# Kernel optimization log

Hardware: AMD Instinct MI355X
Metric: run time of the kernel (lower is better)

The kernel has to match this reference:

```python
import jax, jax.numpy as jnp
import numpy as np

DIM = 192
HEADS = 4
EPS = 1e-12  # F.normalize default eps


def setup_inputs() -> dict:
    key = jax.random.key(0)
    k0, k1, k2, k3 = jax.random.split(key, 4)
    x = jax.random.normal(k0, (4, DIM, 128, 128), dtype=jnp.float32)
    # qkv 1x1 conv weight: [3*dim, dim, 1, 1] -> stored as [3*dim, dim]
    w_qkv = jax.random.normal(k1, (3 * DIM, DIM), dtype=jnp.float32) * (1.0 / np.sqrt(DIM))
    # depthwise 3x3 conv weight: [3*dim, 1, 3, 3]
    w_dw = jax.random.normal(k2, (3 * DIM, 1, 3, 3), dtype=jnp.float32) * (1.0 / 3.0)
    # project_out 1x1 conv weight: [dim, dim]
    w_proj = jax.random.normal(k3, (DIM, DIM), dtype=jnp.float32) * (1.0 / np.sqrt(DIM))
    # temperature: ones(heads,1,1), requires_grad=False in original
    temperature = jnp.ones((HEADS, 1, 1), dtype=jnp.float32)
    return {"x": x, "w_qkv": w_qkv, "w_dw": w_dw, "w_proj": w_proj,
            "temperature": temperature}


def _l2norm(t):
    # F.normalize(t, dim=-1): t / max(||t||_2, eps)
    n = jnp.sqrt(jnp.sum(t * t, axis=-1, keepdims=True))
    return t / jnp.maximum(n, EPS)


def reference(x, w_qkv, w_dw, w_proj, temperature):
    b, c, h, w = x.shape
    ch = c // HEADS  # channels per head
    # 1x1 conv (no bias) == channel GEMM
    qkv = jnp.einsum('oc,bchw->bohw', w_qkv, x)
    # depthwise 3x3 conv, padding=1, groups=3*dim
    qkv = jax.lax.conv_general_dilated(
        qkv, w_dw, window_strides=(1, 1), padding=((1, 1), (1, 1)),
        dimension_numbers=('NCHW', 'OIHW', 'NCHW'),
        feature_group_count=3 * c)
    q, k, v = jnp.split(qkv, 3, axis=1)
    # b (head ch) h w -> b head ch (h w)
    def rearr(t):
        return t.reshape(b, HEADS, ch, h * w)
    q, k, v = rearr(q), rearr(k), rearr(v)
    q = _l2norm(q)
    k = _l2norm(k)
    # channel-channel attention: [b, head, ch, ch]
    attn = jnp.einsum('bhcn,bhdn->bhcd', q, k) * temperature[None]
    attn = jax.nn.softmax(attn, axis=-1)
    out = jnp.einsum('bhcd,bhdn->bhcn', attn, v)
    out = out.reshape(b, c, h, w)
    out = jnp.einsum('oc,bchw->bohw', w_proj, out)
    return out
```

## Files before the change

kernel.cpp:

```cpp
#include <hip/hip_runtime.h>

typedef unsigned short u16;
typedef float f32x4 __attribute__((ext_vector_type(4)));
typedef __bf16 bf16x8 __attribute__((ext_vector_type(8)));
typedef unsigned short u16x8 __attribute__((ext_vector_type(8)));
typedef unsigned short u16x4 __attribute__((ext_vector_type(4)));

#define DEV static __device__ __forceinline__

#define QS 16448

DEV u16 f2bf(float f) {
  unsigned int u = __float_as_uint(f);
  u += 0x7FFFu + ((u >> 16) & 1u);
  return (u16)(u >> 16);
}
DEV float bf2f(u16 h) { return __uint_as_float(((unsigned int)h) << 16); }

DEV void gload_lds16(const void* g, void* l) {
  __builtin_amdgcn_global_load_lds(
      (__attribute__((address_space(1))) void*)(unsigned long long)g,
      (__attribute__((address_space(3))) void*)l, 16, 0, 0);
}

DEV void vm_wait(int n) {
  switch (n) {
    case 0:  asm volatile("s_waitcnt vmcnt(0)" ::: "memory"); break;
    case 2:  asm volatile("s_waitcnt vmcnt(2)" ::: "memory"); break;
    case 4:  asm volatile("s_waitcnt vmcnt(4)" ::: "memory"); break;
    case 6:  asm volatile("s_waitcnt vmcnt(6)" ::: "memory"); break;
    case 8:  asm volatile("s_waitcnt vmcnt(8)" ::: "memory"); break;
    case 10: asm volatile("s_waitcnt vmcnt(10)" ::: "memory"); break;
    default: asm volatile("s_waitcnt vmcnt(14)" ::: "memory"); break;
  }
}

__global__ __launch_bounds__(256) void convert_w_kernel(
    const float* __restrict__ in, u16* __restrict__ out, int n) {
  int i = blockIdx.x * 256 + threadIdx.x;
  if (i < n) out[i] = f2bf(in[i]);
}

template <bool IN_F32, bool OUT_BF16, int NJT>
__global__ __launch_bounds__(256, 2) void gemm_bt_kernel(
    const void* __restrict__ Av, const u16* __restrict__ B,
    void* __restrict__ Cv, size_t aBatch, int aStride, size_t bBatch,
    size_t cBatch, int ldC) {
  __shared__ __align__(16) char smem[73728];
  char* sA = smem;

  const int tid = threadIdx.x, wave = tid >> 6, lane = tid & 63;
  const int m0 = blockIdx.x * 64, b = blockIdx.y;
  const char* Bbase = (const char*)(B + (size_t)b * bBatch);
  char* bufs = smem + 24576 + wave * 12288;
  const int jwbase = wave * (NJT * 16);
  constexpr int S = OUT_BF16 ? 2 : 4;

  f32x4 vaf[3][4];
  u16x8 vau[2][4];
  if (IN_F32) {
    const float* Xb = (const float*)Av + (size_t)b * aBatch + m0;
    const int cbl = tid & 15, iq = tid >> 4;
#pragma unroll
    for (int p = 0; p < 3; ++p)
#pragma unroll
      for (int r = 0; r < 4; ++r)
        vaf[p][r] = *(const f32x4*)(Xb + (size_t)((p * 16 + cbl) * 4 + r) *
                                             aStride + iq * 4);
  } else {
    const u16* Vb = (const u16*)Av + (size_t)b * aBatch + m0;
#pragma unroll
    for (int p = 0; p < 2; ++p) {
      const int task = p * 256 + tid;
      if (task < 384) {
        const int cb = task >> 3, io = task & 7;
#pragma unroll
        for (int r = 0; r < 4; ++r)
          vau[p][r] = *(const u16x8*)(Vb + (size_t)(cb * 4 + r) * aStride +
                                      io * 8);
      }
    }
  }
#pragma unroll
  for (int t = 0; t < 2; ++t) {
    if (t < NJT) {
#pragma unroll
      for (int i = 0; i < 6; ++i) {
        const int d = i * 1024 + lane * 16;
        const int row = d / 384, inrow = d - row * 384;
        gload_lds16(Bbase + (size_t)(jwbase + t * 16 + row) * 384 +
                        (inrow ^ ((row & 7) << 4)),
                    bufs + t * 6144 + i * 1024);
      }
    }
  }
  if (IN_F32) {
    const int cbl = tid & 15, iq = tid >> 4;
#pragma unroll
    for (int p = 0; p < 3; ++p) {
      const int cb = p * 16 + cbl;
#pragma unroll
      for (int j = 0; j < 4; ++j) {
        const int n = iq * 4 + j;
        u16x4 col;
        col[0] = f2bf(vaf[p][0][j]);
        col[1] = f2bf(vaf[p][1][j]);
        col[2] = f2bf(vaf[p][2][j]);
        col[3] = f2bf(vaf[p][3][j]);
        *(u16x4*)(sA + n * 384 + ((cb * 8) ^ ((n & 7) << 4))) = col;
      }
    }
  } else {
#pragma unroll
    for (int p = 0; p < 2; ++p) {
      const int task = p * 256 + tid;
      if (task < 384) {
        const int cb = task >> 3, io = task & 7;
#pragma unroll
        for (int j = 0; j < 8; ++j) {
          const int n = io * 8 + j;
          u16x4 col;
          col[0] = vau[p][0][j];
          col[1] = vau[p][1][j];
          col[2] = vau[p][2][j];
          col[3] = vau[p][3][j];
          *(u16x4*)(sA + n * 384 + ((cb * 8) ^ ((n & 7) << 4))) = col;
        }
      }
    }
  }
  asm volatile("s_waitcnt lgkmcnt(0)" ::: "memory");
  __builtin_amdgcn_s_barrier();

  const int l15 = lane & 15, lg = lane >> 4;
  const int swm = (l15 & 7) << 4;

  bf16x8 af[4][6];
#pragma unroll
  for (int mi = 0; mi < 4; ++mi)
#pragma unroll
    for (int ks = 0; ks < 6; ++ks)
      af[mi][ks] = *(const bf16x8*)(sA + (mi * 16 + l15) * 384 +
                                    ((ks * 64 + lg * 16) ^ swm));
  asm volatile("s_waitcnt lgkmcnt(0)" ::: "memory");
  __builtin_amdgcn_s_barrier();

  char* rbuf = sA + wave * 6144;

#pragma unroll
  for (int t = 0; t < NJT; ++t) {
    vm_wait(t == 0 ? (NJT > 1 ? 6 : 0) : (S + (t + 1 < NJT ? 6 : 0)));
    __builtin_amdgcn_sched_barrier(0);
    char* bw = bufs + (t & 1) * 6144;
    bf16x8 bfv[6];
#pragma unroll
    for (int ks = 0; ks < 6; ++ks)
      bfv[ks] = *(const bf16x8*)(bw + l15 * 384 + ((ks * 64 + lg * 16) ^ swm));
    f32x4 acc[4];
#pragma unroll
    for (int mi = 0; mi < 4; ++mi) acc[mi] = (f32x4){0.f, 0.f, 0.f, 0.f};
#pragma unroll
    for (int ks = 0; ks < 6; ++ks)
#pragma unroll
      for (int mi = 0; mi < 4; ++mi)
        acc[mi] = __builtin_amdgcn_mfma_f32_16x16x32_bf16(af[mi][ks], bfv[ks],
                                                          acc[mi], 0, 0, 0);
    if (OUT_BF16) {
#pragma unroll
      for (int mi = 0; mi < 4; ++mi) {
        u16x4 ov;
#pragma unroll
        for (int r = 0; r < 4; ++r) ov[r] = f2bf(acc[mi][r]);
        *(u16x4*)(rbuf + l15 * 136 + mi * 32 + lg * 8) = ov;
      }
      asm volatile("s_waitcnt lgkmcnt(0)" ::: "memory");
      u16* Cb = (u16*)Cv + (size_t)b * cBatch;
#pragma unroll
      for (int half = 0; half < 2; ++half) {
        const int row = half * 8 + (lane >> 3);
        const u16x8 val = *(const u16x8*)(rbuf + row * 136 + (lane & 7) * 16);
        *(u16x8*)(Cb + (size_t)(jwbase + t * 16 + row) * ldC + m0 +
                  (lane & 7) * 8) = val;
      }
    } else {
#pragma unroll
      for (int mi = 0; mi < 4; ++mi)
        *(f32x4*)(rbuf + l15 * 272 + mi * 64 + lg * 16) = acc[mi];
      asm volatile("s_waitcnt lgkmcnt(0)" ::: "memory");
      float* Cb = (float*)Cv + (size_t)b * cBatch;
#pragma unroll
      for (int q = 0; q < 4; ++q) {
        const int row = q * 4 + (lane >> 4);
        const f32x4 val = *(const f32x4*)(rbuf + row * 272 + (lane & 15) * 16);
        *(f32x4*)(Cb + (size_t)(jwbase + t * 16 + row) * ldC + m0 +
                  (lane & 15) * 4) = val;
      }
    }
    if (t + 2 < NJT) {
      __builtin_amdgcn_sched_barrier(0);
#pragma unroll
      for (int i = 0; i < 6; ++i) {
        const int d = i * 1024 + lane * 16;
        const int row = d / 384, inrow = d - row * 384;
        gload_lds16(Bbase + (size_t)(jwbase + (t + 2) * 16 + row) * 384 +
                        (inrow ^ ((row & 7) << 4)),
                    bw + i * 1024);
      }
    }
  }
}

__global__ __launch_bounds__(256) void dwconv_kernel(
    u16* __restrict__ qkv, const float* __restrict__ wdw,
    float* __restrict__ sq) {
  __shared__ u16 img[16384];
  __shared__ float red[4];
  const int o = blockIdx.x, b = blockIdx.y;
  const size_t base = ((size_t)b * 576 + o) * QS;
  const int tid = threadIdx.x, wave = tid >> 6, lane = tid & 63;
#pragma unroll
  for (int i = 0; i < 8; ++i) {
    const int off = (i * 4 + wave) * 1024;
    gload_lds16((const char*)qkv + base * 2 + off + lane * 16, (char*)img + off);
  }
  asm volatile("s_waitcnt vmcnt(0)" ::: "memory");
  __syncthreads();
  float w[9];
#pragma unroll
  for (int j = 0; j < 9; ++j) w[j] = wdw[o * 9 + j];
  float sqacc = 0.f;
  for (int it = 0; it < 8; ++it) {
    const int chunk = it * 256 + tid;
    const int px0 = chunk * 8;
    const int y = px0 >> 7, x0 = px0 & 127;
    float acc[8];
#pragma unroll
    for (int j = 0; j < 8; ++j) acc[j] = 0.f;
#pragma unroll
    for (int dy = -1; dy <= 1; ++dy) {
      const int yy = y + dy;
      float v[10];
      if (yy >= 0 && yy <= 127) {
        const u16* rowp = img + yy * 128 + x0;
        u16x8 m = *(const u16x8*)rowp;
#pragma unroll
        for (int j = 0; j < 8; ++j) v[j + 1] = bf2f(m[j]);
        v[0] = (x0 > 0) ? bf2f(rowp[-1]) : 0.f;
        v[9] = (x0 < 120) ? bf2f(rowp[8]) : 0.f;
      } else {
#pragma unroll
        for (int j = 0; j < 10; ++j) v[j] = 0.f;
      }
      const float w0 = w[(dy + 1) * 3], w1 = w[(dy + 1) * 3 + 1],
                  w2 = w[(dy + 1) * 3 + 2];
#pragma unroll
      for (int j = 0; j < 8; ++j) acc[j] += w0 * v[j] + w1 * v[j + 1] + w2 * v[j + 2];
    }
    u16x8 ov;
#pragma unroll
    for (int j = 0; j < 8; ++j) {
      sqacc += acc[j] * acc[j];
      ov[j] = f2bf(acc[j]);
    }
    *(u16x8*)(qkv + base + px0) = ov;
  }
#pragma unroll
  for (int s = 32; s > 0; s >>= 1) sqacc += __shfl_xor(sqacc, s, 64);
  if (lane == 0) red[wave] = sqacc;
  __syncthreads();
  if (tid == 0) sq[b * 576 + o] = red[0] + red[1] + red[2] + red[3];
}

__global__ __launch_bounds__(256) void gram_kernel(
    const u16* __restrict__ qkv, float* __restrict__ partial) {
  __shared__ u16 tiles[4 * 3072];
  __shared__ float red[4 * 2304];
  const int bh = blockIdx.y, b = bh >> 2, h = bh & 3;
  const int g = blockIdx.x;
  const int wave = threadIdx.x >> 6, lane = threadIdx.x & 63;
  const int n0 = g * 512 + wave * 128;
  const u16* qb = qkv + ((size_t)b * 576 + h * 48) * QS;
  const u16* kb = qb + (size_t)192 * QS;
  char* tl = (char*)(tiles + wave * 3072);
  const int l15 = lane & 15, lg = lane >> 4;
  const int swz = (l15 & 3) << 4;
  f32x4 acc[3][3];
#pragma unroll
  for (int i = 0; i < 3; ++i)
#pragma unroll
    for (int j = 0; j < 3; ++j) acc[i][j] = (f32x4){0.f, 0.f, 0.f, 0.f};

  for (int ks = 0; ks < 4; ++ks) {
    const int nn = n0 + ks * 32;
    asm volatile("s_waitcnt lgkmcnt(0)" ::: "memory");
#pragma unroll
    for (int i = 0; i < 6; ++i) {
      const int flat = i * 1024 + lane * 16;
      const int row = flat >> 6, colb = flat & 63;
      const u16* src = (row < 48) ? (qb + (size_t)row * QS + nn)
                                  : (kb + (size_t)(row - 48) * QS + nn);
      gload_lds16((const char*)src + (colb ^ ((row & 3) << 4)), tl + i * 1024);
    }
    asm volatile("s_waitcnt vmcnt(0)" ::: "memory");
    bf16x8 qf[3], kf[3];
#pragma unroll
    for (int f = 0; f < 3; ++f) {
      qf[f] = *(const bf16x8*)(tl + (f * 16 + l15) * 64 + ((lg * 16) ^ swz));
      kf[f] = *(const bf16x8*)(tl + (48 + f * 16 + l15) * 64 + ((lg * 16) ^ swz));
    }
#pragma unroll
    for (int i = 0; i < 3; ++i)
#pragma unroll
      for (int j = 0; j < 3; ++j)
        acc[i][j] = __builtin_amdgcn_mfma_f32_16x16x32_bf16(qf[i], kf[j],
                                                            acc[i][j], 0, 0, 0);
  }
  {
    float* rw = red + wave * 2304;
#pragma unroll
    for (int i = 0; i < 3; ++i)
#pragma unroll
      for (int j = 0; j < 3; ++j)
#pragma unroll
        for (int r = 0; r < 4; ++r)
          rw[(i * 16 + lg * 4 + r) * 48 + (j * 16 + l15)] = acc[i][j][r];
  }
  __syncthreads();
#pragma unroll
  for (int it = 0; it < 9; ++it) {
    const int p = it * 256 + threadIdx.x;
    const float s = red[p] + red[2304 + p] + red[4608 + p] + red[6912 + p];
    partial[((size_t)bh * 2304 + p) * 32 + g] = s;
  }
}

__global__ __launch_bounds__(256) void reduce_partial_kernel(
    const float* __restrict__ partial, float* __restrict__ G) {
  const int idx = blockIdx.x * 256 + threadIdx.x;
  const f32x4* pp = (const f32x4*)(partial + (size_t)idx * 32);
  const f32x4 a = (pp[0] + pp[1]) + (pp[2] + pp[3]) +
                  (pp[4] + pp[5]) + (pp[6] + pp[7]);
  G[idx] = a.x + a.y + a.z + a.w;
}

__global__ __launch_bounds__(256) void softmax_weff_kernel(
    const float* __restrict__ Gin, const float* __restrict__ sq,
    const float* __restrict__ temp, const float* __restrict__ wproj,
    u16* __restrict__ weff) {
  __shared__ float G[2304];
  __shared__ float wp[192 * 49];
  __shared__ float nq[48], nk[48];
  const int bh = blockIdx.x, b = bh >> 2, h = bh & 3;
  const int tid = threadIdx.x;
#pragma unroll
  for (int it = 0; it < 36; ++it) {
    const int j = it * 256 + tid;
    const int o = j / 48, c = j - o * 48;
    wp[o * 49 + c] = wproj[o * 192 + h * 48 + c];
  }
#pragma unroll
  for (int it = 0; it < 9; ++it) {
    const int p = it * 256 + tid;
    G[p] = Gin[(size_t)bh * 2304 + p];
  }
  if (tid < 48) {
    nq[tid] = fmaxf(sqrtf(sq[b * 576 + h * 48 + tid]), 1e-12f);
    nk[tid] = fmaxf(sqrtf(sq[b * 576 + 192 + h * 48 + tid]), 1e-12f);
  }
  __syncthreads();
  if (tid < 48) {
    const int r = tid;
    const float inq = temp[h] / nq[r];
    float L[48];
    float mx = -3.4e38f;
#pragma unroll 4
    for (int d = 0; d < 48; ++d) {
      const float v = G[r * 48 + d] * inq / nk[d];
      L[d] = v;
      mx = fmaxf(mx, v);
    }
    float s = 0.f;
#pragma unroll 4
    for (int d = 0; d < 48; ++d) {
      const float e = __expf(L[d] - mx);
      L[d] = e;
      s += e;
    }
    const float inv = 1.f / s;
#pragma unroll 4
    for (int d = 0; d < 48; ++d) G[r * 48 + d] = L[d] * inv;
  }
  __syncthreads();
  if (tid < 192) {
    const int o = tid;
    f32x4 acc[12];
#pragma unroll
    for (int dv = 0; dv < 12; ++dv) acc[dv] = (f32x4){0.f, 0.f, 0.f, 0.f};
    for (int c = 0; c < 48; ++c) {
      const float w = wp[o * 49 + c];
      const f32x4* at = (const f32x4*)(G + c * 48);
#pragma unroll
      for (int dv = 0; dv < 12; ++dv) acc[dv] += w * at[dv];
    }
    u16* op = weff + ((size_t)b * 192 + o) * 192 + h * 48;
#pragma unroll
    for (int g8 = 0; g8 < 6; ++g8) {
      u16x8 ov;
#pragma unroll
      for (int j = 0; j < 8; ++j) {
        const int d = g8 * 8 + j;
        ov[j] = f2bf(acc[d >> 2][d & 3]);
      }
      *(u16x8*)(op + g8 * 8) = ov;
    }
  }
}

extern "C" void kernel_launch(void* const* d_in, const int* in_sizes, int n_in,
                              void* d_out, int out_size, void* d_ws,
                              size_t ws_size, hipStream_t stream) {
  (void)in_sizes; (void)n_in; (void)out_size; (void)ws_size;
  const float* x      = (const float*)d_in[0];
  const float* w_qkv  = (const float*)d_in[1];
  const float* w_dw   = (const float*)d_in[2];
  const float* w_proj = (const float*)d_in[3];
  const float* temp   = (const float*)d_in[4];

  char* ws = (char*)d_ws;
  u16*   qkv     = (u16*)ws;
  float* partial = (float*)(ws + 75792384);
  float* G       = (float*)(ws + 80510976);
  float* sq      = (float*)(ws + 80658432);
  u16*   Wq      = (u16*)(ws + 80667648);
  u16*   Weff    = (u16*)(ws + 80888832);

  convert_w_kernel<<<dim3(432), 256, 0, stream>>>(w_qkv, Wq, 110592);
  gemm_bt_kernel<true, true, 9><<<dim3(256, 4), 256, 0, stream>>>(
      x, Wq, qkv, (size_t)192 * 16384, 16384, 0, (size_t)576 * QS, QS);
  dwconv_kernel<<<dim3(576, 4), 256, 0, stream>>>(qkv, w_dw, sq);
  gram_kernel<<<dim3(32, 16), 256, 0, stream>>>(qkv, partial);
  reduce_partial_kernel<<<dim3(144), 256, 0, stream>>>(partial, G);
  softmax_weff_kernel<<<dim3(16), 256, 0, stream>>>(G, sq, temp, w_proj, Weff);
  gemm_bt_kernel<false, false, 3><<<dim3(256, 4), 256, 0, stream>>>(
      qkv + (size_t)384 * QS, Weff, d_out, (size_t)576 * QS, QS,
      (size_t)192 * 192, (size_t)192 * 16384, 16384);
}
```

Baseline: 135.2 us.

## Pre-transpose x to bf16 and split GEMMs into small per-tile workgroups

Adds a transpose kernel that converts x to a bf16 pixel-major layout, staged in the output buffer, so the QKV GEMM can load A tiles straight into LDS. Both GEMMs are replaced by one-tile-per-workgroup kernels (9216 and 3072 blocks) with an XCD-aware block remap, smaller LDS and three blocks per CU, instead of looping over N tiles with double buffering. The aim is more parallelism and less in-kernel conversion work, at the cost of an extra kernel and an extra round trip of the transposed input through memory, with A tiles reloaded once per output-channel tile.

Measured after the change: 154.5 us. 14.3% more time.

```diff
diff --git a/kernel.cpp b/kernel.cpp
--- a/kernel.cpp
+++ b/kernel.cpp
@@ -23,190 +23,190 @@
       (__attribute__((address_space(3))) void*)l, 16, 0, 0);
 }
 
-DEV void vm_wait(int n) {
-  switch (n) {
-    case 0:  asm volatile("s_waitcnt vmcnt(0)" ::: "memory"); break;
-    case 2:  asm volatile("s_waitcnt vmcnt(2)" ::: "memory"); break;
-    case 4:  asm volatile("s_waitcnt vmcnt(4)" ::: "memory"); break;
-    case 6:  asm volatile("s_waitcnt vmcnt(6)" ::: "memory"); break;
-    case 8:  asm volatile("s_waitcnt vmcnt(8)" ::: "memory"); break;
-    case 10: asm volatile("s_waitcnt vmcnt(10)" ::: "memory"); break;
-    default: asm volatile("s_waitcnt vmcnt(14)" ::: "memory"); break;
-  }
-}
-
 __global__ __launch_bounds__(256) void convert_w_kernel(
     const float* __restrict__ in, u16* __restrict__ out, int n) {
   int i = blockIdx.x * 256 + threadIdx.x;
   if (i < n) out[i] = f2bf(in[i]);
 }
 
-template <bool IN_F32, bool OUT_BF16, int NJT>
-__global__ __launch_bounds__(256, 2) void gemm_bt_kernel(
-    const void* __restrict__ Av, const u16* __restrict__ B,
-    void* __restrict__ Cv, size_t aBatch, int aStride, size_t bBatch,
-    size_t cBatch, int ldC) {
-  __shared__ __align__(16) char smem[73728];
+__global__ __launch_bounds__(256) void transpose_f32_kernel(
+    const float* __restrict__ in, u16* __restrict__ out) {
+  __shared__ u16 ls[64][66];
+  const int b = blockIdx.z;
+  const int c0 = blockIdx.x * 64, r0 = blockIdx.y * 64;
+  const float* ip = in + (size_t)b * 192 * 16384;
+  u16* op = out + (size_t)b * 16384 * 192;
+  const int t = threadIdx.x;
+  const int rr = t >> 4, cg = t & 15;
+#pragma unroll
+  for (int i = 0; i < 4; ++i) {
+    const int r = i * 16 + rr;
+    const f32x4 v = *(const f32x4*)(ip + (size_t)(r0 + r) * 16384 + c0 + cg * 4);
+    ls[r][cg * 4 + 0] = f2bf(v.x);
+    ls[r][cg * 4 + 1] = f2bf(v.y);
+    ls[r][cg * 4 + 2] = f2bf(v.z);
+    ls[r][cg * 4 + 3] = f2bf(v.w);
+  }
+  __syncthreads();
+  const int lane = t & 63, w = t >> 6;
+#pragma unroll
+  for (int i = 0; i < 16; ++i) {
+    const int c = i * 4 + w;
+    op[(size_t)(c0 + c) * 192 + r0 + lane] = ls[lane][c];
+  }
+}
+
+__global__ __launch_bounds__(256, 3) void gemm_xt_kernel(
+    const u16* __restrict__ Xt, const u16* __restrict__ W,
+    u16* __restrict__ C, int nwg) {
+  __shared__ __align__(16) char smem[49152];
   char* sA = smem;
-
   const int tid = threadIdx.x, wave = tid >> 6, lane = tid & 63;
-  const int m0 = blockIdx.x * 64, b = blockIdx.y;
-  const char* Bbase = (const char*)(B + (size_t)b * bBatch);
-  char* bufs = smem + 24576 + wave * 12288;
-  const int jwbase = wave * (NJT * 16);
-  constexpr int S = OUT_BF16 ? 2 : 4;
-
-  f32x4 vaf[3][4];
+  char* sBw = smem + 24576 + wave * 6144;
+
+  const int p = blockIdx.x;
+  const int id = (p & 7) * (nwg >> 3) + (p >> 3);
+  const int j = id % 9;
+  const int t = id / 9;
+  const int m0 = (t & 255) * 64, b = t >> 8;
+
+  const char* Ab = (const char*)(Xt + ((size_t)b * 16384 + m0) * 192);
+  const char* Bb = (const char*)(W + (size_t)(j * 64 + wave * 16) * 192);
+
+#pragma unroll
+  for (int i = 0; i < 6; ++i) {
+    const int c = i * 4 + wave;
+    const int d = c * 1024 + lane * 16;
+    const int row = d / 384, inrow = d - row * 384;
+    gload_lds16(Ab + row * 384 + (inrow ^ ((row & 7) << 4)), sA + c * 1024);
+  }
+#pragma unroll
+  for (int i = 0; i < 6; ++i) {
+    const int d = i * 1024 + lane * 16;
+    const int row = d / 384, inrow = d - row * 384;
+    gload_lds16(Bb + row * 384 + (inrow ^ ((row & 7) << 4)), sBw + i * 1024);
+  }
+  asm volatile("s_waitcnt vmcnt(0)" ::: "memory");
+  __builtin_amdgcn_s_barrier();
+
+  const int l15 = lane & 15, lg = lane >> 4;
+  const int swm = (l15 & 7) << 4;
+
+  f32x4 acc[4];
+#pragma unroll
+  for (int mi = 0; mi < 4; ++mi) acc[mi] = (f32x4){0.f, 0.f, 0.f, 0.f};
+#pragma unroll
+  for (int ks = 0; ks < 6; ++ks) {
+    const int col = (ks * 64 + lg * 16) ^ swm;
+    const bf16x8 bv = *(const bf16x8*)(sBw + l15 * 384 + col);
+#pragma unroll
+    for (int mi = 0; mi < 4; ++mi) {
+      const bf16x8 av = *(const bf16x8*)(sA + (mi * 16 + l15) * 384 + col);
+      acc[mi] = __builtin_amdgcn_mfma_f32_16x16x32_bf16(av, bv, acc[mi], 0, 0, 0);
+    }
+  }
+  asm volatile("s_waitcnt lgkmcnt(0)" ::: "memory");
+#pragma unroll
+  for (int mi = 0; mi < 4; ++mi) {
+    u16x4 ov;
+#pragma unroll
+    for (int r = 0; r < 4; ++r) ov[r] = f2bf(acc[mi][r]);
+    *(u16x4*)(sBw + l15 * 136 + mi * 32 + lg * 8) = ov;
+  }
+  asm volatile("s_waitcnt lgkmcnt(0)" ::: "memory");
+  u16* Cb = C + (size_t)b * 576 * QS;
+  const int jrow0 = j * 64 + wave * 16;
+#pragma unroll
+  for (int half = 0; half < 2; ++half) {
+    const int row = half * 8 + (lane >> 3);
+    const u16x8 val = *(const u16x8*)(sBw + row * 136 + (lane & 7) * 16);
+    *(u16x8*)(Cb + (size_t)(jrow0 + row) * QS + m0 + (lane & 7) * 8) = val;
+  }
+}
+
+__global__ __launch_bounds__(256, 3) void gemm_v_kernel(
+    const u16* __restrict__ V, const u16* __restrict__ Weff,
+    float* __restrict__ C, int nwg) {
+  __shared__ __align__(16) char smem[49152];
+  char* sA = smem;
+  const int tid = threadIdx.x, wave = tid >> 6, lane = tid & 63;
+  char* sBw = smem + 24576 + wave * 6144;
+
+  const int p = blockIdx.x;
+  const int id = (p & 7) * (nwg >> 3) + (p >> 3);
+  const int j = id % 3;
+  const int t = id / 3;
+  const int m0 = (t & 255) * 64, b = t >> 8;
+
+  const u16* Vb = V + (size_t)b * 576 * QS + m0;
+  const char* Bb = (const char*)(Weff + (size_t)b * 192 * 192 +
+                                 (size_t)(j * 64 + wave * 16) * 192);
+
   u16x8 vau[2][4];
-  if (IN_F32) {
-    const float* Xb = (const float*)Av + (size_t)b * aBatch + m0;
-    const int cbl = tid & 15, iq = tid >> 4;
-#pragma unroll
-    for (int p = 0; p < 3; ++p)
+#pragma unroll
+  for (int pp = 0; pp < 2; ++pp) {
+    const int task = pp * 256 + tid;
+    if (task < 384) {
+      const int cb = task >> 3, io = task & 7;
 #pragma unroll
       for (int r = 0; r < 4; ++r)
-        vaf[p][r] = *(const f32x4*)(Xb + (size_t)((p * 16 + cbl) * 4 + r) *
-                                             aStride + iq * 4);
-  } else {
-    const u16* Vb = (const u16*)Av + (size_t)b * aBatch + m0;
-#pragma unroll
-    for (int p = 0; p < 2; ++p) {
-      const int task = p * 256 + tid;
-      if (task < 384) {
-        const int cb = task >> 3, io = task & 7;
-#pragma unroll
-        for (int r = 0; r < 4; ++r)
-          vau[p][r] = *(const u16x8*)(Vb + (size_t)(cb * 4 + r) * aStride +
-                                      io * 8);
-      }
-    }
-  }
-#pragma unroll
-  for (int t = 0; t < 2; ++t) {
-    if (t < NJT) {
-#pragma unroll
-      for (int i = 0; i < 6; ++i) {
-        const int d = i * 1024 + lane * 16;
-        const int row = d / 384, inrow = d - row * 384;
-        gload_lds16(Bbase + (size_t)(jwbase + t * 16 + row) * 384 +
-                        (inrow ^ ((row & 7) << 4)),
-                    bufs + t * 6144 + i * 1024);
-      }
-    }
-  }
-  if (IN_F32) {
-    const int cbl = tid & 15, iq = tid >> 4;
-#pragma unroll
-    for (int p = 0; p < 3; ++p) {
-      const int cb = p * 16 + cbl;
-#pragma unroll
-      for (int j = 0; j < 4; ++j) {
-        const int n = iq * 4 + j;
+        vau[pp][r] = *(const u16x8*)(Vb + (size_t)(cb * 4 + r) * QS + io * 8);
+    }
+  }
+#pragma unroll
+  for (int i = 0; i < 6; ++i) {
+    const int d = i * 1024 + lane * 16;
+    const int row = d / 384, inrow = d - row * 384;
+    gload_lds16(Bb + row * 384 + (inrow ^ ((row & 7) << 4)), sBw + i * 1024);
+  }
+#pragma unroll
+  for (int pp = 0; pp < 2; ++pp) {
+    const int task = pp * 256 + tid;
+    if (task < 384) {
+      const int cb = task >> 3, io = task & 7;
+#pragma unroll
+      for (int q = 0; q < 8; ++q) {
+        const int n = io * 8 + q;
         u16x4 col;
-        col[0] = f2bf(vaf[p][0][j]);
-        col[1] = f2bf(vaf[p][1][j]);
-        col[2] = f2bf(vaf[p][2][j]);
-        col[3] = f2bf(vaf[p][3][j]);
+        col[0] = vau[pp][0][q];
+        col[1] = vau[pp][1][q];
+        col[2] = vau[pp][2][q];
+        col[3] = vau[pp][3][q];
         *(u16x4*)(sA + n * 384 + ((cb * 8) ^ ((n & 7) << 4))) = col;
       }
     }
-  } else {
-#pragma unroll
-    for (int p = 0; p < 2; ++p) {
-      const int task = p * 256 + tid;
-      if (task < 384) {
-        const int cb = task >> 3, io = task & 7;
-#pragma unroll
-        for (int j = 0; j < 8; ++j) {
-          const int n = io * 8 + j;
-          u16x4 col;
-          col[0] = vau[p][0][j];
-          col[1] = vau[p][1][j];
-          col[2] = vau[p][2][j];
-          col[3] = vau[p][3][j];
-          *(u16x4*)(sA + n * 384 + ((cb * 8) ^ ((n & 7) << 4))) = col;
-        }
-      }
-    }
-  }
-  asm volatile("s_waitcnt lgkmcnt(0)" ::: "memory");
+  }
+  asm volatile("s_waitcnt vmcnt(0) lgkmcnt(0)" ::: "memory");
   __builtin_amdgcn_s_barrier();
 
   const int l15 = lane & 15, lg = lane >> 4;
   const int swm = (l15 & 7) << 4;
 
-  bf16x8 af[4][6];
+  f32x4 acc[4];
+#pragma unroll
+  for (int mi = 0; mi < 4; ++mi) acc[mi] = (f32x4){0.f, 0.f, 0.f, 0.f};
+#pragma unroll
+  for (int ks = 0; ks < 6; ++ks) {
+    const int col = (ks * 64 + lg * 16) ^ swm;
+    const bf16x8 bv = *(const bf16x8*)(sBw + l15 * 384 + col);
+#pragma unroll
+    for (int mi = 0; mi < 4; ++mi) {
+      const bf16x8 av = *(const bf16x8*)(sA + (mi * 16 + l15) * 384 + col);
+      acc[mi] = __builtin_amdgcn_mfma_f32_16x16x32_bf16(av, bv, acc[mi], 0, 0, 0);
+    }
+  }
+  asm volatile("s_waitcnt lgkmcnt(0)" ::: "memory");
 #pragma unroll
   for (int mi = 0; mi < 4; ++mi)
-#pragma unroll
-    for (int ks = 0; ks < 6; ++ks)
-      af[mi][ks] = *(const bf16x8*)(sA + (mi * 16 + l15) * 384 +
-                                    ((ks * 64 + lg * 16) ^ swm));
+    *(f32x4*)(sBw + l15 * 272 + mi * 64 + lg * 16) = acc[mi];
   asm volatile("s_waitcnt lgkmcnt(0)" ::: "memory");
-  __builtin_amdgcn_s_barrier();
-
-  char* rbuf = sA + wave * 6144;
-
-#pragma unroll
-  for (int t = 0; t < NJT; ++t) {
-    vm_wait(t == 0 ? (NJT > 1 ? 6 : 0) : (S + (t + 1 < NJT ? 6 : 0)));
-    __builtin_amdgcn_sched_barrier(0);
-    char* bw = bufs + (t & 1) * 6144;
-    bf16x8 bfv[6];
-#pragma unroll
-    for (int ks = 0; ks < 6; ++ks)
-      bfv[ks] = *(const bf16x8*)(bw + l15 * 384 + ((ks * 64 + lg * 16) ^ swm));
-    f32x4 acc[4];
-#pragma unroll
-    for (int mi = 0; mi < 4; ++mi) acc[mi] = (f32x4){0.f, 0.f, 0.f, 0.f};
-#pragma unroll
-    for (int ks = 0; ks < 6; ++ks)
-#pragma unroll
-      for (int mi = 0; mi < 4; ++mi)
-        acc[mi] = __builtin_amdgcn_mfma_f32_16x16x32_bf16(af[mi][ks], bfv[ks],
-                                                          acc[mi], 0, 0, 0);
-    if (OUT_BF16) {
-#pragma unroll
-      for (int mi = 0; mi < 4; ++mi) {
-        u16x4 ov;
-#pragma unroll
-        for (int r = 0; r < 4; ++r) ov[r] = f2bf(acc[mi][r]);
-        *(u16x4*)(rbuf + l15 * 136 + mi * 32 + lg * 8) = ov;
-      }
-      asm volatile("s_waitcnt lgkmcnt(0)" ::: "memory");
-      u16* Cb = (u16*)Cv + (size_t)b * cBatch;
-#pragma unroll
-      for (int half = 0; half < 2; ++half) {
-        const int row = half * 8 + (lane >> 3);
-        const u16x8 val = *(const u16x8*)(rbuf + row * 136 + (lane & 7) * 16);
-        *(u16x8*)(Cb + (size_t)(jwbase + t * 16 + row) * ldC + m0 +
-                  (lane & 7) * 8) = val;
-      }
-    } else {
-#pragma unroll
-      for (int mi = 0; mi < 4; ++mi)
-        *(f32x4*)(rbuf + l15 * 272 + mi * 64 + lg * 16) = acc[mi];
-      asm volatile("s_waitcnt lgkmcnt(0)" ::: "memory");
-      float* Cb = (float*)Cv + (size_t)b * cBatch;
-#pragma unroll
-      for (int q = 0; q < 4; ++q) {
-        const int row = q * 4 + (lane >> 4);
-        const f32x4 val = *(const f32x4*)(rbuf + row * 272 + (lane & 15) * 16);
-        *(f32x4*)(Cb + (size_t)(jwbase + t * 16 + row) * ldC + m0 +
-                  (lane & 15) * 4) = val;
-      }
-    }
-    if (t + 2 < NJT) {
-      __builtin_amdgcn_sched_barrier(0);
-#pragma unroll
-      for (int i = 0; i < 6; ++i) {
-        const int d = i * 1024 + lane * 16;
-        const int row = d / 384, inrow = d - row * 384;
-        gload_lds16(Bbase + (size_t)(jwbase + (t + 2) * 16 + row) * 384 +
-                        (inrow ^ ((row & 7) << 4)),
-                    bw + i * 1024);
-      }
-    }
+  float* Cb = C + (size_t)b * 192 * 16384;
+  const int jrow0 = j * 64 + wave * 16;
+#pragma unroll
+  for (int q = 0; q < 4; ++q) {
+    const int row = q * 4 + (lane >> 4);
+    const f32x4 val = *(const f32x4*)(sBw + row * 272 + (lane & 15) * 16);
+    *(f32x4*)(Cb + (size_t)(jrow0 + row) * 16384 + m0 + (lane & 15) * 4) = val;
   }
 }
 
@@ -433,15 +433,15 @@
   float* sq      = (float*)(ws + 80658432);
   u16*   Wq      = (u16*)(ws + 80667648);
   u16*   Weff    = (u16*)(ws + 80888832);
+  u16*   Xt      = (u16*)d_out;
 
   convert_w_kernel<<<dim3(432), 256, 0, stream>>>(w_qkv, Wq, 110592);
-  gemm_bt_kernel<true, true, 9><<<dim3(256, 4), 256, 0, stream>>>(
-      x, Wq, qkv, (size_t)192 * 16384, 16384, 0, (size_t)576 * QS, QS);
+  transpose_f32_kernel<<<dim3(256, 3, 4), 256, 0, stream>>>(x, Xt);
+  gemm_xt_kernel<<<dim3(9216), 256, 0, stream>>>(Xt, Wq, qkv, 9216);
   dwconv_kernel<<<dim3(576, 4), 256, 0, stream>>>(qkv, w_dw, sq);
   gram_kernel<<<dim3(32, 16), 256, 0, stream>>>(qkv, partial);
   reduce_partial_kernel<<<dim3(144), 256, 0, stream>>>(partial, G);
   softmax_weff_kernel<<<dim3(16), 256, 0, stream>>>(G, sq, temp, w_proj, Weff);
-  gemm_bt_kernel<false, false, 3><<<dim3(256, 4), 256, 0, stream>>>(
-      qkv + (size_t)384 * QS, Weff, d_out, (size_t)576 * QS, QS,
-      (size_t)192 * 192, (size_t)192 * 16384, 16384);
-}
+  gemm_v_kernel<<<dim3(3072), 256, 0, stream>>>(qkv + (size_t)384 * QS, Weff,
+                                                (float*)d_out, 3072);
+}
```

## Halve GEMM spatial tile to 32 columns and double grid size

Applied to the files above, without the earlier changes.

Cuts the per-block spatial tile of both 1x1-conv GEMMs from 64 to 32 columns and launches twice as many blocks. The A staging loads, LDS layout, MFMA accumulator count, epilogue store pattern and vmcnt wait counts are all resized to match. The goal is more blocks per GPU and less LDS per block for better occupancy and latency hiding. In exchange, each block reloads the full weight tile for half the output work, which doubles weight traffic and per-block overhead.

Measured after the change: 146.6 us. 1.08x slower.

```diff
diff --git a/kernel.cpp b/kernel.cpp
--- a/kernel.cpp
+++ b/kernel.cpp
@@ -26,11 +26,11 @@
 DEV void vm_wait(int n) {
   switch (n) {
     case 0:  asm volatile("s_waitcnt vmcnt(0)" ::: "memory"); break;
+    case 1:  asm volatile("s_waitcnt vmcnt(1)" ::: "memory"); break;
     case 2:  asm volatile("s_waitcnt vmcnt(2)" ::: "memory"); break;
-    case 4:  asm volatile("s_waitcnt vmcnt(4)" ::: "memory"); break;
     case 6:  asm volatile("s_waitcnt vmcnt(6)" ::: "memory"); break;
+    case 7:  asm volatile("s_waitcnt vmcnt(7)" ::: "memory"); break;
     case 8:  asm volatile("s_waitcnt vmcnt(8)" ::: "memory"); break;
-    case 10: asm volatile("s_waitcnt vmcnt(10)" ::: "memory"); break;
     default: asm volatile("s_waitcnt vmcnt(14)" ::: "memory"); break;
   }
 }
@@ -46,29 +46,20 @@
     const void* __restrict__ Av, const u16* __restrict__ B,
     void* __restrict__ Cv, size_t aBatch, int aStride, size_t bBatch,
     size_t cBatch, int ldC) {
-  __shared__ __align__(16) char smem[73728];
+  __shared__ __align__(16) char smem[61440];
   char* sA = smem;
 
   const int tid = threadIdx.x, wave = tid >> 6, lane = tid & 63;
-  const int m0 = blockIdx.x * 64, b = blockIdx.y;
+  const int m0 = blockIdx.x * 32, b = blockIdx.y;
   const char* Bbase = (const char*)(B + (size_t)b * bBatch);
-  char* bufs = smem + 24576 + wave * 12288;
+  char* bufs = smem + 12288 + wave * 12288;
   const int jwbase = wave * (NJT * 16);
-  constexpr int S = OUT_BF16 ? 2 : 4;
-
-  f32x4 vaf[3][4];
-  u16x8 vau[2][4];
+  constexpr int S = OUT_BF16 ? 1 : 2;
+
+  f32x4 vaf[2][4];
+  u16x8 vau[4];
   if (IN_F32) {
     const float* Xb = (const float*)Av + (size_t)b * aBatch + m0;
-    const int cbl = tid & 15, iq = tid >> 4;
-#pragma unroll
-    for (int p = 0; p < 3; ++p)
-#pragma unroll
-      for (int r = 0; r < 4; ++r)
-        vaf[p][r] = *(const f32x4*)(Xb + (size_t)((p * 16 + cbl) * 4 + r) *
-                                             aStride + iq * 4);
-  } else {
-    const u16* Vb = (const u16*)Av + (size_t)b * aBatch + m0;
 #pragma unroll
     for (int p = 0; p < 2; ++p) {
       const int task = p * 256 + tid;
@@ -76,9 +67,17 @@
         const int cb = task >> 3, io = task & 7;
 #pragma unroll
         for (int r = 0; r < 4; ++r)
-          vau[p][r] = *(const u16x8*)(Vb + (size_t)(cb * 4 + r) * aStride +
-                                      io * 8);
-      }
+          vaf[p][r] = *(const f32x4*)(Xb + (size_t)(cb * 4 + r) * aStride +
+                                      io * 4);
+      }
+    }
+  } else {
+    const u16* Vb = (const u16*)Av + (size_t)b * aBatch + m0;
+    if (tid < 192) {
+      const int cb = tid >> 2, io = tid & 3;
+#pragma unroll
+      for (int r = 0; r < 4; ++r)
+        vau[r] = *(const u16x8*)(Vb + (size_t)(cb * 4 + r) * aStride + io * 8);
     }
   }
 #pragma unroll
@@ -95,39 +94,37 @@
     }
   }
   if (IN_F32) {
-    const int cbl = tid & 15, iq = tid >> 4;
-#pragma unroll
-    for (int p = 0; p < 3; ++p) {
-      const int cb = p * 16 + cbl;
-#pragma unroll
-      for (int j = 0; j < 4; ++j) {
-        const int n = iq * 4 + j;
-        u16x4 col;
-        col[0] = f2bf(vaf[p][0][j]);
-        col[1] = f2bf(vaf[p][1][j]);
-        col[2] = f2bf(vaf[p][2][j]);
-        col[3] = f2bf(vaf[p][3][j]);
-        *(u16x4*)(sA + n * 384 + ((cb * 8) ^ ((n & 7) << 4))) = col;
-      }
-    }
-  } else {
 #pragma unroll
     for (int p = 0; p < 2; ++p) {
       const int task = p * 256 + tid;
       if (task < 384) {
         const int cb = task >> 3, io = task & 7;
 #pragma unroll
-        for (int j = 0; j < 8; ++j) {
-          const int n = io * 8 + j;
+        for (int j = 0; j < 4; ++j) {
+          const int n = io * 4 + j;
           u16x4 col;
-          col[0] = vau[p][0][j];
-          col[1] = vau[p][1][j];
-          col[2] = vau[p][2][j];
-          col[3] = vau[p][3][j];
+          col[0] = f2bf(vaf[p][0][j]);
+          col[1] = f2bf(vaf[p][1][j]);
+          col[2] = f2bf(vaf[p][2][j]);
+          col[3] = f2bf(vaf[p][3][j]);
           *(u16x4*)(sA + n * 384 + ((cb * 8) ^ ((n & 7) << 4))) = col;
         }
       }
     }
+  } else {
+    if (tid < 192) {
+      const int cb = tid >> 2, io = tid & 3;
+#pragma unroll
+      for (int j = 0; j < 8; ++j) {
+        const int n = io * 8 + j;
+        u16x4 col;
+        col[0] = vau[0][j];
+        col[1] = vau[1][j];
+        col[2] = vau[2][j];
+        col[3] = vau[3][j];
+        *(u16x4*)(sA + n * 384 + ((cb * 8) ^ ((n & 7) << 4))) = col;
+      }
+    }
   }
   asm volatile("s_waitcnt lgkmcnt(0)" ::: "memory");
   __builtin_amdgcn_s_barrier();
@@ -135,9 +132,9 @@
   const int l15 = lane & 15, lg = lane >> 4;
   const int swm = (l15 & 7) << 4;
 
-  bf16x8 af[4][6];
-#pragma unroll
-  for (int mi = 0; mi < 4; ++mi)
+  bf16x8 af[2][6];
+#pragma unroll
+  for (int mi = 0; mi < 2; ++mi)
 #pragma unroll
     for (int ks = 0; ks < 6; ++ks)
       af[mi][ks] = *(const bf16x8*)(sA + (mi * 16 + l15) * 384 +
@@ -145,7 +142,7 @@
   asm volatile("s_waitcnt lgkmcnt(0)" ::: "memory");
   __builtin_amdgcn_s_barrier();
 
-  char* rbuf = sA + wave * 6144;
+  char* rbuf = sA + wave * 3072;
 
 #pragma unroll
   for (int t = 0; t < NJT; ++t) {
@@ -156,44 +153,42 @@
 #pragma unroll
     for (int ks = 0; ks < 6; ++ks)
       bfv[ks] = *(const bf16x8*)(bw + l15 * 384 + ((ks * 64 + lg * 16) ^ swm));
-    f32x4 acc[4];
-#pragma unroll
-    for (int mi = 0; mi < 4; ++mi) acc[mi] = (f32x4){0.f, 0.f, 0.f, 0.f};
+    f32x4 acc[2];
+#pragma unroll
+    for (int mi = 0; mi < 2; ++mi) acc[mi] = (f32x4){0.f, 0.f, 0.f, 0.f};
 #pragma unroll
     for (int ks = 0; ks < 6; ++ks)
 #pragma unroll
-      for (int mi = 0; mi < 4; ++mi)
+      for (int mi = 0; mi < 2; ++mi)
         acc[mi] = __builtin_amdgcn_mfma_f32_16x16x32_bf16(af[mi][ks], bfv[ks],
                                                           acc[mi], 0, 0, 0);
+    const int jrow0 = jwbase + t * 16;
     if (OUT_BF16) {
 #pragma unroll
-      for (int mi = 0; mi < 4; ++mi) {
+      for (int mi = 0; mi < 2; ++mi) {
         u16x4 ov;
 #pragma unroll
         for (int r = 0; r < 4; ++r) ov[r] = f2bf(acc[mi][r]);
-        *(u16x4*)(rbuf + l15 * 136 + mi * 32 + lg * 8) = ov;
+        *(u16x4*)(rbuf + l15 * 72 + mi * 32 + lg * 8) = ov;
       }
       asm volatile("s_waitcnt lgkmcnt(0)" ::: "memory");
       u16* Cb = (u16*)Cv + (size_t)b * cBatch;
-#pragma unroll
-      for (int half = 0; half < 2; ++half) {
-        const int row = half * 8 + (lane >> 3);
-        const u16x8 val = *(const u16x8*)(rbuf + row * 136 + (lane & 7) * 16);
-        *(u16x8*)(Cb + (size_t)(jwbase + t * 16 + row) * ldC + m0 +
-                  (lane & 7) * 8) = val;
+      {
+        const int row = lane >> 2;
+        const u16x8 val = *(const u16x8*)(rbuf + row * 72 + (lane & 3) * 16);
+        *(u16x8*)(Cb + (size_t)(jrow0 + row) * ldC + m0 + (lane & 3) * 8) = val;
       }
     } else {
 #pragma unroll
-      for (int mi = 0; mi < 4; ++mi)
-        *(f32x4*)(rbuf + l15 * 272 + mi * 64 + lg * 16) = acc[mi];
+      for (int mi = 0; mi < 2; ++mi)
+        *(f32x4*)(rbuf + l15 * 144 + mi * 64 + lg * 16) = acc[mi];
       asm volatile("s_waitcnt lgkmcnt(0)" ::: "memory");
       float* Cb = (float*)Cv + (size_t)b * cBatch;
 #pragma unroll
-      for (int q = 0; q < 4; ++q) {
-        const int row = q * 4 + (lane >> 4);
-        const f32x4 val = *(const f32x4*)(rbuf + row * 272 + (lane & 15) * 16);
-        *(f32x4*)(Cb + (size_t)(jwbase + t * 16 + row) * ldC + m0 +
-                  (lane & 15) * 4) = val;
+      for (int q = 0; q < 2; ++q) {
+        const int row = q * 8 + (lane >> 3);
+        const f32x4 val = *(const f32x4*)(rbuf + row * 144 + (lane & 7) * 16);
+        *(f32x4*)(Cb + (size_t)(jrow0 + row) * ldC + m0 + (lane & 7) * 4) = val;
       }
     }
     if (t + 2 < NJT) {
@@ -435,13 +430,13 @@
   u16*   Weff    = (u16*)(ws + 80888832);
 
   convert_w_kernel<<<dim3(432), 256, 0, stream>>>(w_qkv, Wq, 110592);
-  gemm_bt_kernel<true, true, 9><<<dim3(256, 4), 256, 0, stream>>>(
+  gemm_bt_kernel<true, true, 9><<<dim3(512, 4), 256, 0, stream>>>(
       x, Wq, qkv, (size_t)192 * 16384, 16384, 0, (size_t)576 * QS, QS);
   dwconv_kernel<<<dim3(576, 4), 256, 0, stream>>>(qkv, w_dw, sq);
   gram_kernel<<<dim3(32, 16), 256, 0, stream>>>(qkv, partial);
   reduce_partial_kernel<<<dim3(144), 256, 0, stream>>>(partial, G);
   softmax_weff_kernel<<<dim3(16), 256, 0, stream>>>(G, sq, temp, w_proj, Weff);
-  gemm_bt_kernel<false, false, 3><<<dim3(256, 4), 256, 0, stream>>>(
+  gemm_bt_kernel<false, false, 3><<<dim3(512, 4), 256, 0, stream>>>(
       qkv + (size_t)384 * QS, Weff, d_out, (size_t)576 * QS, QS,
       (size_t)192 * 192, (size_t)192 * 16384, 16384);
 }
```
